# Performance work log

Hardware: AMD Instinct MI355X
Metric: run time of the kernel (lower is better)

## Reference

```python
import jax, jax.numpy as jnp
import numpy as np

IN_F = 1024
OUT_F = 1024
B, S = 8, 4096


def _pack_ternary(tern):
    # encoding: -1 -> 0, 0 -> 1, +1 -> 2; 4 values per byte, matching torch pack_ternary_weights
    enc = (tern + 1.0).astype(jnp.int32).reshape(-1)  # length divisible by 4 here
    return (enc[0::4] | (enc[1::4] << 2) | (enc[2::4] << 4) | (enc[3::4] << 6)).astype(jnp.int32)


def setup_inputs() -> dict:
    key = jax.random.key(0)
    kx, kw = jax.random.split(key)
    x = jax.random.normal(kx, (B, S, IN_F), dtype=jnp.float32)
    w = jax.random.normal(kw, (OUT_F, IN_F), dtype=jnp.float32) * 0.02
    # quantize_weights_158bit
    scale = jnp.maximum(jnp.mean(jnp.abs(w)), 1e-5)
    wn = w / scale
    tern = jnp.sign(wn) * (jnp.abs(wn) > 0.5).astype(jnp.float32)
    packed = _pack_ternary(tern)
    bias = jnp.zeros((OUT_F,), dtype=jnp.float32)
    return {"x": x, "packed_weight": packed, "weight_scale": scale.reshape(1), "bias": bias}


def reference(x, packed_weight, weight_scale, bias):
    n = OUT_F * IN_F
    shifts = jnp.array([0, 2, 4, 6], dtype=jnp.int32)
    # Faithful to original unpack_ternary_weights: concatenate bit-planes, then truncate.
    # (This is a permutation of the packed order, replicated deliberately.)
    enc = ((packed_weight[None, :] >> shifts[:, None]) & 3).reshape(-1)[:n]
    w = (enc.astype(jnp.float32) - 1.0).reshape(OUT_F, IN_F) * weight_scale  # dequant ternary
    # training path: INT8 per-token activation fake-quant
    act_scale = 127.0 / jnp.maximum(jnp.max(jnp.abs(x), axis=-1, keepdims=True), 1e-5)
    x_dq = jnp.clip(jnp.round(x * act_scale), -128.0, 127.0) / act_scale
    return jnp.einsum('bsi,oi->bso', x_dq, w) + bias
```

## Files before the change

### kernel.cpp

```cpp
#include <hip/hip_runtime.h>
#include <hip/hip_bf16.h>
#include <stdint.h>

typedef int i32x4 __attribute__((ext_vector_type(4)));

constexpr int IN_F = 1024;
constexpr int OUT_F = 1024;
constexpr int M_TOT = 8 * 4096;
constexpr int K_TOT = IN_F;
constexpr int N_TOT = OUT_F;

__global__ __launch_bounds__(256) void quant_kernel(
    const float* __restrict__ x,
    const float* __restrict__ wscale,
    int8_t* __restrict__ q,
    float* __restrict__ inv_row)
{
    const int row = blockIdx.x;
    const int t = threadIdx.x;
    const float4 v = reinterpret_cast<const float4*>(x + (size_t)row * IN_F)[t];
    float m = fmaxf(fmaxf(fabsf(v.x), fabsf(v.y)), fmaxf(fabsf(v.z), fabsf(v.w)));
    #pragma unroll
    for (int off = 32; off > 0; off >>= 1)
        m = fmaxf(m, __shfl_xor(m, off));
    __shared__ float smax[4];
    if ((t & 63) == 0) smax[t >> 6] = m;
    __syncthreads();
    m = fmaxf(fmaxf(smax[0], smax[1]), fmaxf(smax[2], smax[3]));
    const float a = fmaxf(m, 1e-5f);
    const float as = 127.0f / a;

    char4 o;
    o.x = (char)(int)fminf(fmaxf(rintf(v.x * as), -128.0f), 127.0f);
    o.y = (char)(int)fminf(fmaxf(rintf(v.y * as), -128.0f), 127.0f);
    o.z = (char)(int)fminf(fmaxf(rintf(v.z * as), -128.0f), 127.0f);
    o.w = (char)(int)fminf(fmaxf(rintf(v.w * as), -128.0f), 127.0f);
    reinterpret_cast<char4*>(q + (size_t)row * IN_F)[t] = o;
    if (t == 0) inv_row[row] = (a / 127.0f) * wscale[0];
}

__global__ __launch_bounds__(256) void unpack_kernel(
    const int* __restrict__ packed,
    int8_t* __restrict__ wt)
{
    const int o = blockIdx.x;
    const int k0 = threadIdx.x * 4;
    const int sh = (o >> 8) * 2;
    const int pbase = ((o & 255) << 10) + k0;
    const int4 pw = *reinterpret_cast<const int4*>(packed + pbase);
    char4 r;
    r.x = (char)(((pw.x >> sh) & 3) - 1);
    r.y = (char)(((pw.y >> sh) & 3) - 1);
    r.z = (char)(((pw.z >> sh) & 3) - 1);
    r.w = (char)(((pw.w >> sh) & 3) - 1);
    *reinterpret_cast<char4*>(wt + (size_t)o * IN_F + k0) = r;
}

constexpr int BM = 256, BN = 128, BK = 64;
constexpr int NT = K_TOT / BK;

__global__ __launch_bounds__(512, 4) void gemm_kernel(
    const int8_t* __restrict__ qa,
    const int8_t* __restrict__ wb,
    const float* __restrict__ inv_row,
    const float* __restrict__ bias,
    float* __restrict__ out)
{
    int bid = blockIdx.x;
    bid = (bid & 7) * ((int)gridDim.x >> 3) + (bid >> 3);
    const int tm = bid >> 3;
    const int tn = bid & 7;

    const int tid = threadIdx.x;
    const int lane = tid & 63;
    const int wid = tid >> 6;
    const int wr = wid >> 1;
    const int wc = wid & 1;

    __shared__ int8_t ldsA[3 * 256 * 64];
    __shared__ int8_t ldsB[3 * 128 * 64];

    const int rowA0 = tm * BM;
    const int rowB0 = tn * BN;
    const int frow = lane & 15;
    const int fq = lane >> 4;

    i32x4 acc[4][4] = {};

    const int r0 = tid >> 2;
    const int scc0 = (tid & 3) ^ ((r0 >> 1) & 3);
    const int8_t* srcA0 = qa + (size_t)(rowA0 + r0) * K_TOT + scc0 * 16;
    const int8_t* srcB0 = wb + (size_t)(rowB0 + r0) * K_TOT + scc0 * 16;
    const int dA0 = tid * 16, dA1 = (512 + tid) * 16;

    auto stage = [&](int slot, int kt) {
        __builtin_amdgcn_global_load_lds(
            (const __attribute__((address_space(1))) void*)(srcA0 + kt * BK),
            (__attribute__((address_space(3))) void*)&ldsA[slot * 16384 + dA0], 16, 0, 0);
        __builtin_amdgcn_global_load_lds(
            (const __attribute__((address_space(1))) void*)(srcA0 + (size_t)128 * K_TOT + kt * BK),
            (__attribute__((address_space(3))) void*)&ldsA[slot * 16384 + dA1], 16, 0, 0);
        __builtin_amdgcn_global_load_lds(
            (const __attribute__((address_space(1))) void*)(srcB0 + kt * BK),
            (__attribute__((address_space(3))) void*)&ldsB[slot * 8192 + dA0], 16, 0, 0);
    };

    auto ldA = [&](int slot, int mf) -> i32x4 {
        const int r = wr * 64 + mf * 16 + frow;
        const int ch = fq ^ ((r >> 1) & 3);
        return *reinterpret_cast<const i32x4*>(&ldsA[slot * 16384 + r * 64 + ch * 16]);
    };
    auto ldB = [&](int slot, int nf) -> i32x4 {
        const int r = wc * 64 + nf * 16 + frow;
        const int ch = fq ^ ((r >> 1) & 3);
        return *reinterpret_cast<const i32x4*>(&ldsB[slot * 8192 + r * 64 + ch * 16]);
    };

    stage(0, 0);
    stage(1, 1);

    int sCur = 0;
    for (int T = 0; T < NT; ++T) {
        const int s = sCur;
        const int s2 = (sCur + 2 >= 3) ? sCur - 1 : sCur + 2;

        if (T < NT - 1) asm volatile("s_waitcnt vmcnt(3)" ::: "memory");
        else            asm volatile("s_waitcnt vmcnt(0)" ::: "memory");
        __builtin_amdgcn_s_barrier();

        i32x4 aF[4], bF[4];
        #pragma unroll
        for (int mf = 0; mf < 4; ++mf) aF[mf] = ldA(s, mf);
        #pragma unroll
        for (int nf = 0; nf < 4; ++nf) bF[nf] = ldB(s, nf);

        if (T + 2 < NT) stage(s2, T + 2);

        asm volatile("s_waitcnt lgkmcnt(0)" ::: "memory");
        __builtin_amdgcn_sched_barrier(0);
        __builtin_amdgcn_s_setprio(1);
        #pragma unroll
        for (int mf = 0; mf < 4; ++mf)
            #pragma unroll
            for (int nf = 0; nf < 4; ++nf)
                acc[mf][nf] = __builtin_amdgcn_mfma_i32_16x16x64_i8(
                    aF[mf], bF[nf], acc[mf][nf], 0, 0, 0);
        __builtin_amdgcn_s_setprio(0);

        sCur = (sCur + 1 >= 3) ? 0 : sCur + 1;
    }

    #pragma unroll
    for (int mf = 0; mf < 4; ++mf) {
        #pragma unroll
        for (int j = 0; j < 4; ++j) {
            const int gm = rowA0 + wr * 64 + mf * 16 + fq * 4 + j;
            const float sc = inv_row[gm];
            #pragma unroll
            for (int nf = 0; nf < 4; ++nf) {
                const int gn = rowB0 + wc * 64 + nf * 16 + frow;
                out[(size_t)gm * N_TOT + gn] = (float)acc[mf][nf][j] * sc + bias[gn];
            }
        }
    }
}

extern "C" void kernel_launch(void* const* d_in, const int* in_sizes, int n_in,
                              void* d_out, int out_size, void* d_ws, size_t ws_size,
                              hipStream_t stream) {
    const float* x = (const float*)d_in[0];
    const int* packed = (const int*)d_in[1];
    const float* wscale = (const float*)d_in[2];
    const float* bias = (const float*)d_in[3];
    float* out = (float*)d_out;

    int8_t* q = (int8_t*)d_ws;
    int8_t* wt = (int8_t*)((char*)d_ws + (size_t)M_TOT * K_TOT);
    float* inv_row = (float*)((char*)d_ws + (size_t)M_TOT * K_TOT + (size_t)N_TOT * K_TOT);

    quant_kernel<<<M_TOT, 256, 0, stream>>>(x, wscale, q, inv_row);
    unpack_kernel<<<OUT_F, 256, 0, stream>>>(packed, wt);
    gemm_kernel<<<(M_TOT / BM) * (N_TOT / BN), 512, 0, stream>>>(q, wt, inv_row, bias, out);
}
```

Baseline: 89.57 us.

## Load B fragments directly from global in pre-tiled layout, bypassing LDS

The unpack kernel now writes weights in a K-tile-major layout, so each MFMA B fragment is a contiguous 16-byte global load. The GEMM drops the B LDS buffer and loads B fragments straight into registers, double-buffered two tiles ahead, with the vmcnt waits adjusted. The aim is to cut LDS traffic and LDS footprint for B. In exchange it adds per-wave global loads that are not shared across waves, plus more register pressure.

```diff
diff --git a/kernel.cpp b/kernel.cpp
--- a/kernel.cpp
+++ b/kernel.cpp
@@ -41,10 +41,11 @@
 
 __global__ __launch_bounds__(256) void unpack_kernel(
     const int* __restrict__ packed,
-    int8_t* __restrict__ wt)
+    int8_t* __restrict__ wt2)
 {
     const int o = blockIdx.x;
-    const int k0 = threadIdx.x * 4;
+    const int t = threadIdx.x;
+    const int k0 = t * 4;
     const int sh = (o >> 8) * 2;
     const int pbase = ((o & 255) << 10) + k0;
     const int4 pw = *reinterpret_cast<const int4*>(packed + pbase);
@@ -53,7 +54,8 @@
     r.y = (char)(((pw.y >> sh) & 3) - 1);
     r.z = (char)(((pw.z >> sh) & 3) - 1);
     r.w = (char)(((pw.w >> sh) & 3) - 1);
-    *reinterpret_cast<char4*>(wt + (size_t)o * IN_F + k0) = r;
+    const int addr = (k0 >> 6) * 65536 + o * 64 + ((k0 >> 4) & 3) * 16 + (k0 & 15);
+    *reinterpret_cast<char4*>(wt2 + addr) = r;
 }
 
 constexpr int BM = 256, BN = 128, BK = 64;
@@ -61,7 +63,7 @@
 
 __global__ __launch_bounds__(512, 4) void gemm_kernel(
     const int8_t* __restrict__ qa,
-    const int8_t* __restrict__ wb,
+    const int8_t* __restrict__ wb2,
     const float* __restrict__ inv_row,
     const float* __restrict__ bias,
     float* __restrict__ out)
@@ -78,7 +80,6 @@
     const int wc = wid & 1;
 
     __shared__ int8_t ldsA[3 * 256 * 64];
-    __shared__ int8_t ldsB[3 * 128 * 64];
 
     const int rowA0 = tm * BM;
     const int rowB0 = tn * BN;
@@ -90,19 +91,15 @@
     const int r0 = tid >> 2;
     const int scc0 = (tid & 3) ^ ((r0 >> 1) & 3);
     const int8_t* srcA0 = qa + (size_t)(rowA0 + r0) * K_TOT + scc0 * 16;
-    const int8_t* srcB0 = wb + (size_t)(rowB0 + r0) * K_TOT + scc0 * 16;
     const int dA0 = tid * 16, dA1 = (512 + tid) * 16;
 
-    auto stage = [&](int slot, int kt) {
+    auto stageA = [&](int slot, int kt) {
         __builtin_amdgcn_global_load_lds(
             (const __attribute__((address_space(1))) void*)(srcA0 + kt * BK),
             (__attribute__((address_space(3))) void*)&ldsA[slot * 16384 + dA0], 16, 0, 0);
         __builtin_amdgcn_global_load_lds(
             (const __attribute__((address_space(1))) void*)(srcA0 + (size_t)128 * K_TOT + kt * BK),
             (__attribute__((address_space(3))) void*)&ldsA[slot * 16384 + dA1], 16, 0, 0);
-        __builtin_amdgcn_global_load_lds(
-            (const __attribute__((address_space(1))) void*)(srcB0 + kt * BK),
-            (__attribute__((address_space(3))) void*)&ldsB[slot * 8192 + dA0], 16, 0, 0);
     };
 
     auto ldA = [&](int slot, int mf) -> i32x4 {
@@ -110,31 +107,32 @@
         const int ch = fq ^ ((r >> 1) & 3);
         return *reinterpret_cast<const i32x4*>(&ldsA[slot * 16384 + r * 64 + ch * 16]);
     };
-    auto ldB = [&](int slot, int nf) -> i32x4 {
-        const int r = wc * 64 + nf * 16 + frow;
-        const int ch = fq ^ ((r >> 1) & 3);
-        return *reinterpret_cast<const i32x4*>(&ldsB[slot * 8192 + r * 64 + ch * 16]);
+
+    const int8_t* wbBase = wb2 + (size_t)(rowB0 + wc * 64 + frow) * 64 + fq * 16;
+    auto loadB = [&](int kt, i32x4 (&b)[4]) {
+        #pragma unroll
+        for (int nf = 0; nf < 4; ++nf)
+            b[nf] = *reinterpret_cast<const i32x4*>(wbBase + kt * 65536 + nf * 1024);
     };
 
-    stage(0, 0);
-    stage(1, 1);
+    i32x4 bX[4], bY[4];
 
-    int sCur = 0;
-    for (int T = 0; T < NT; ++T) {
-        const int s = sCur;
-        const int s2 = (sCur + 2 >= 3) ? sCur - 1 : sCur + 2;
+    stageA(0, 0);
+    stageA(1, 1);
+    loadB(0, bX);
+    loadB(1, bY);
 
-        if (T < NT - 1) asm volatile("s_waitcnt vmcnt(3)" ::: "memory");
-        else            asm volatile("s_waitcnt vmcnt(0)" ::: "memory");
+    auto body = [&](int T, i32x4 (&bCur)[4]) {
+        const int s = T % 3;
+        if (T < NT - 1) asm volatile("s_waitcnt vmcnt(10)" ::: "memory");
+        else            asm volatile("s_waitcnt vmcnt(4)" ::: "memory");
         __builtin_amdgcn_s_barrier();
 
-        i32x4 aF[4], bF[4];
+        i32x4 aF[4];
         #pragma unroll
         for (int mf = 0; mf < 4; ++mf) aF[mf] = ldA(s, mf);
-        #pragma unroll
-        for (int nf = 0; nf < 4; ++nf) bF[nf] = ldB(s, nf);
 
-        if (T + 2 < NT) stage(s2, T + 2);
+        if (T + 2 < NT) stageA((T + 2) % 3, T + 2);
 
         asm volatile("s_waitcnt lgkmcnt(0)" ::: "memory");
         __builtin_amdgcn_sched_barrier(0);
@@ -144,10 +142,15 @@
             #pragma unroll
             for (int nf = 0; nf < 4; ++nf)
                 acc[mf][nf] = __builtin_amdgcn_mfma_i32_16x16x64_i8(
-                    aF[mf], bF[nf], acc[mf][nf], 0, 0, 0);
+                    aF[mf], bCur[nf], acc[mf][nf], 0, 0, 0);
         __builtin_amdgcn_s_setprio(0);
 
-        sCur = (sCur + 1 >= 3) ? 0 : sCur + 1;
+        if (T + 2 < NT) loadB(T + 2, bCur);
+    };
+
+    for (int t2 = 0; t2 < NT; t2 += 2) {
+        body(t2, bX);
+        body(t2 + 1, bY);
     }
 
     #pragma unroll
@@ -175,10 +178,10 @@
     float* out = (float*)d_out;
 
     int8_t* q = (int8_t*)d_ws;
-    int8_t* wt = (int8_t*)((char*)d_ws + (size_t)M_TOT * K_TOT);
+    int8_t* wt2 = (int8_t*)((char*)d_ws + (size_t)M_TOT * K_TOT);
     float* inv_row = (float*)((char*)d_ws + (size_t)M_TOT * K_TOT + (size_t)N_TOT * K_TOT);
 
     quant_kernel<<<M_TOT, 256, 0, stream>>>(x, wscale, q, inv_row);
-    unpack_kernel<<<OUT_F, 256, 0, stream>>>(packed, wt);
-    gemm_kernel<<<(M_TOT / BM) * (N_TOT / BN), 512, 0, stream>>>(q, wt, inv_row, bias, out);
+    unpack_kernel<<<OUT_F, 256, 0, stream>>>(packed, wt2);
+    gemm_kernel<<<(M_TOT / BM) * (N_TOT / BN), 512, 0, stream>>>(q, wt2, inv_row, bias, out);
 }
```

Result: slower. 98.51 us (+10.0%).
